# Kernel optimization log

Measured on AMD Instinct MI355X. Metric: run time of the kernel, lower is better.

Reference implementation:

```python
import jax, jax.numpy as jnp
import numpy as np

T, R, I = 16384, 1024, 128   # time steps, reservoir size, input size
CONN, SR = 0.05, 0.9         # connectivity_rate, spectral_radius


def _make_reservoir(rng):
    # Faithful to ESN.create_reservoir_weights: uniform[0,1), sparsify by
    # connectivity_rate, rescale to target spectral radius, flip half the
    # entries' signs.
    W = rng.random((R, R)).astype(np.float32)
    W[rng.random((R, R)) > CONN] = 0.0
    cur_sr = np.max(np.abs(np.linalg.eigvals(W)))
    W = W * (SR / cur_sr)
    neg = rng.choice(R * R, (R * R) // 2, replace=False)
    Wf = W.reshape(-1).copy()
    Wf[neg] *= -1.0
    return Wf.reshape(R, R).astype(np.float32)


def setup_inputs() -> dict:
    rng = np.random.default_rng(0)
    W_res = jnp.asarray(_make_reservoir(rng))
    key = jax.random.key(0)
    k1, k2 = jax.random.split(key)
    X = jax.random.normal(k1, (T, I), dtype=jnp.float32)
    # nn.init.uniform_(w, a=-1, b=1)
    W_in = jax.random.uniform(k2, (R, I), dtype=jnp.float32, minval=-1.0, maxval=1.0)
    state0 = jnp.zeros((R,), dtype=jnp.float32)
    return {"X": X, "W_in": W_in, "W_res": W_res, "state0": state0}


def reference(X, W_in, W_res, state0):
    # state_t = tanh(W_in @ x_t + W_res @ state_{t-1}); collect all states (T, R).
    # Input projections are independent across time -> one big GEMM up front.
    U = X @ W_in.T  # (T, R)

    def step(s, u):
        s = jnp.tanh(u + W_res @ s)
        return s, s

    _, all_states = jax.lax.scan(step, state0, U)
    return all_states  # (T, R), matches update_state's all_states
```

## Files before the change

kernel.cpp:

```cpp
#include <hip/hip_runtime.h>
#include <hip/hip_bf16.h>
#include <stdint.h>


constexpr int T_N = 16384;
constexpr int R_N = 1024;
constexpr int I_N = 128;

constexpr int BT = 64, BR = 64;

__global__ __launch_bounds__(256) void gemm_u_kernel(
    const float* __restrict__ X, const float* __restrict__ Win,
    float* __restrict__ U)
{
    __shared__ float XS[BT][68];
    __shared__ float WS[BR][68];
    const int tid = threadIdx.x;
    const int ty = tid >> 4, tx = tid & 15;
    const int t0 = blockIdx.x * BT;
    const int r0 = blockIdx.y * BR;
    float acc[4][4] = {};

    for (int k0 = 0; k0 < I_N; k0 += 64) {
        for (int idx = tid; idx < BT * 16; idx += 256) {
            int row = idx >> 4, c4 = (idx & 15) << 2;
            *reinterpret_cast<float4*>(&XS[row][c4]) =
                *reinterpret_cast<const float4*>(&X[(size_t)(t0 + row) * I_N + k0 + c4]);
        }
        for (int idx = tid; idx < BR * 16; idx += 256) {
            int row = idx >> 4, c4 = (idx & 15) << 2;
            *reinterpret_cast<float4*>(&WS[row][c4]) =
                *reinterpret_cast<const float4*>(&Win[(size_t)(r0 + row) * I_N + k0 + c4]);
        }
        __syncthreads();
#pragma unroll
        for (int k = 0; k < 64; k += 4) {
            float4 a[4], b[4];
#pragma unroll
            for (int i = 0; i < 4; ++i)
                a[i] = *reinterpret_cast<const float4*>(&XS[ty + 16 * i][k]);
#pragma unroll
            for (int jj = 0; jj < 4; ++jj)
                b[jj] = *reinterpret_cast<const float4*>(&WS[tx + 16 * jj][k]);
#pragma unroll
            for (int i = 0; i < 4; ++i)
#pragma unroll
                for (int jj = 0; jj < 4; ++jj)
                    acc[i][jj] += a[i].x * b[jj].x + a[i].y * b[jj].y +
                                  a[i].z * b[jj].z + a[i].w * b[jj].w;
        }
        __syncthreads();
    }
#pragma unroll
    for (int i = 0; i < 4; ++i)
#pragma unroll
        for (int jj = 0; jj < 4; ++jj)
            U[(size_t)(t0 + ty + 16 * i) * R_N + (r0 + tx + 16 * jj)] = acc[i][jj];
}

constexpr int GBLK  = 8;
constexpr int B2    = 1024;
constexpr int RPB   = R_N / GBLK;
constexpr int TPR   = 8;
constexpr int KMAX  = 96;
constexpr int NSL   = KMAX / TPR;
constexpr int DEPTH = 2;
constexpr int PCAP  = 1 << 20;

typedef unsigned long long ull;

__device__ __forceinline__ float fast_tanh(float x) {
    float ax = fabsf(x);
    float e  = __expf(-2.0f * ax);
    float y  = (1.0f - e) / (1.0f + e);
    return copysignf(y, x);
}

__global__ __launch_bounds__(1024) void esn_scan_kernel(
    const float* __restrict__ Wres, const float* __restrict__ state0,
    float* out, ull* slots)
{
    __shared__ float sbuf[DEPTH][R_N];
    __shared__ uint2 ell[RPB][KMAX];
    __shared__ int   cnt[RPB];

    const int tid  = threadIdx.x;
    const int b    = blockIdx.x;
    const int row0 = b * RPB;

    if (tid < RPB) cnt[tid] = 0;
    __syncthreads();
    for (int idx = tid; idx < RPB * R_N; idx += B2) {
        int r = idx >> 10, c = idx & (R_N - 1);
        float w = Wres[(size_t)(row0 + r) * R_N + c];
        if (w != 0.0f) {
            int slot = atomicAdd(&cnt[r], 1);
            if (slot < KMAX) ell[r][slot] = make_uint2((uint32_t)c, __float_as_uint(w));
        }
    }
    __syncthreads();

    const int rloc = tid / TPR;
    const int j    = tid % TPR;
    const int row  = row0 + rloc;
    int   cols[NSL];
    float vals[NSL];
    {
        int myn = cnt[rloc];
#pragma unroll
        for (int k = 0; k < NSL; ++k) {
            int slot = j + k * TPR;
            if (slot < myn) {
                uint2 e = ell[rloc][slot];
                cols[k] = (int)e.x;
                vals[k] = __uint_as_float(e.y);
            } else { cols[k] = 0; vals[k] = 0.0f; }
        }
    }

    sbuf[1][tid] = state0[tid];

    float u_cur = (j == 0) ? out[row] : 0.0f;
    __syncthreads();

    for (int t = 0; t < T_N; ++t) {
        const int p = (t - 1) & 1;

        float u_next = 0.0f;
        if (j == 0 && t + 1 < T_N) u_next = out[(size_t)(t + 1) * R_N + row];

        if (t > 0) {
            const ull* addr = slots + ((size_t)p << 10) + tid;
            const uint32_t want = (uint32_t)t;
            ull w;
            int rounds = 0;
            do {
                w = __hip_atomic_load(addr, __ATOMIC_RELAXED,
                                      __HIP_MEMORY_SCOPE_AGENT);
            } while ((uint32_t)(w >> 32) < want && ++rounds < PCAP);
            sbuf[p][tid] = __uint_as_float((uint32_t)w);
        }
        __syncthreads();

        float acc = 0.0f;
#pragma unroll
        for (int k = 0; k < NSL; ++k) acc += vals[k] * sbuf[p][cols[k]];

        acc += __shfl_xor(acc, 1, TPR);
        acc += __shfl_xor(acc, 2, TPR);
        acc += __shfl_xor(acc, 4, TPR);

        if (j == 0) {
            float y = fast_tanh(u_cur + acc);
            ull pkt = ((ull)(uint32_t)(t + 1) << 32) | (ull)__float_as_uint(y);
            __hip_atomic_store(&slots[((size_t)(t & 1) << 10) + row], pkt,
                               __ATOMIC_RELAXED, __HIP_MEMORY_SCOPE_AGENT);
            out[(size_t)t * R_N + row] = y;
        }
        u_cur = u_next;
    }
}

extern "C" void kernel_launch(void* const* d_in, const int* in_sizes, int n_in,
                              void* d_out, int out_size, void* d_ws, size_t ws_size,
                              hipStream_t stream)
{
    const float* X      = (const float*)d_in[0];
    const float* W_in   = (const float*)d_in[1];
    const float* W_res  = (const float*)d_in[2];
    const float* state0 = (const float*)d_in[3];
    float* out = (float*)d_out;
    ull* slots = (ull*)d_ws;

    hipMemsetAsync(d_ws, 0, (size_t)DEPTH * R_N * sizeof(ull), stream);

    dim3 g1(T_N / BT, R_N / BR);
    gemm_u_kernel<<<g1, 256, 0, stream>>>(X, W_in, out);

    esn_scan_kernel<<<GBLK, B2, 0, stream>>>(W_res, state0, out, slots);
}
```

Measured before the change: 24.27 ms.

## Co-locate scan blocks on one XCD and poll 32-bit tagged slots via L2

The scan kernel now launches 64 blocks and elects the 8 that landed on the same XCD, using the hardware XCC id, to run the recurrence. The other blocks exit. A startup probe checks whether L2 atomic-add reads see peer stores, and if so the per-step handoff polls with those reads. Slots shrink to 32 bits, with an 8-bit step tag packed into the low mantissa bits of the state. The inner sparse loop also skips padded ELL entries. The aim is to cut the per-step cross-block communication latency. The cost is a slightly truncated state value that feeds the recurrence, plus dependence on block placement, with a fallback path when co-location fails.

```diff
diff --git a/kernel.cpp b/kernel.cpp
--- a/kernel.cpp
+++ b/kernel.cpp
@@ -58,16 +58,15 @@
             U[(size_t)(t0 + ty + 16 * i) * R_N + (r0 + tx + 16 * jj)] = acc[i][jj];
 }
 
-constexpr int GBLK  = 8;
-constexpr int B2    = 1024;
-constexpr int RPB   = R_N / GBLK;
-constexpr int TPR   = 8;
-constexpr int KMAX  = 96;
-constexpr int NSL   = KMAX / TPR;
-constexpr int DEPTH = 2;
-constexpr int PCAP  = 1 << 20;
-
-typedef unsigned long long ull;
+constexpr int GBLK    = 8;
+constexpr int NLAUNCH = 64;
+constexpr int B2      = 1024;
+constexpr int RPB     = R_N / GBLK;
+constexpr int TPR     = 8;
+constexpr int KMAX    = 96;
+constexpr int NSL     = KMAX / TPR;
+constexpr int FASTCAP = 24;
+constexpr int PCAP    = 1 << 20;
 
 __device__ __forceinline__ float fast_tanh(float x) {
     float ax = fabsf(x);
@@ -76,17 +75,81 @@
     return copysignf(y, x);
 }
 
+__device__ __forceinline__ uint32_t l2_atomic_read(uint32_t* addr) {
+    uint32_t old;
+    asm volatile("global_atomic_add %0, %1, %2, off sc0\n\t"
+                 "s_waitcnt vmcnt(0)"
+                 : "=v"(old) : "v"(addr), "v"(0u) : "memory");
+    return old;
+}
+
 __global__ __launch_bounds__(1024) void esn_scan_kernel(
     const float* __restrict__ Wres, const float* __restrict__ state0,
-    float* out, ull* slots)
+    float* out, uint32_t* hdr, uint32_t* slots)
 {
-    __shared__ float sbuf[DEPTH][R_N];
+    __shared__ int   s_role, s_fast;
+    __shared__ float sbuf[2][R_N];
     __shared__ uint2 ell[RPB][KMAX];
     __shared__ int   cnt[RPB];
 
-    const int tid  = threadIdx.x;
-    const int b    = blockIdx.x;
+    const int tid = threadIdx.x;
+
+    if (tid == 0) {
+        uint32_t xcd;
+        asm volatile("s_getreg_b32 %0, hwreg(HW_REG_XCC_ID)" : "=s"(xcd));
+        xcd &= 7u;
+        uint32_t rank = __hip_atomic_fetch_add(&hdr[xcd], 1u,
+                            __ATOMIC_RELAXED, __HIP_MEMORY_SCOPE_AGENT);
+        int role = -1;
+        if (rank < (uint32_t)GBLK) {
+            if (rank == (uint32_t)(GBLK - 1)) {
+                uint32_t expected = 0u;
+                __hip_atomic_compare_exchange_strong(&hdr[8], &expected, xcd + 1u,
+                    __ATOMIC_RELAXED, __ATOMIC_RELAXED, __HIP_MEMORY_SCOPE_AGENT);
+            }
+            uint32_t win = 0; int sp = 0;
+            do {
+                win = __hip_atomic_load(&hdr[8], __ATOMIC_RELAXED,
+                                        __HIP_MEMORY_SCOPE_AGENT);
+            } while (win == 0u && ++sp < PCAP);
+            if (win == xcd + 1u) role = (int)rank;
+        }
+        s_role = role; s_fast = 0;
+    }
+    __syncthreads();
+    const int b = s_role;
+    if (b < 0) return;
     const int row0 = b * RPB;
+
+    if (tid == 0) {
+        uint32_t* test = hdr + 96;
+        if (b == 0) {
+            asm volatile("global_store_dword %0, %1, off"
+                         :: "v"(test), "v"(0xC0FFEEu) : "memory");
+            __hip_atomic_store(&hdr[9], 1u, __ATOMIC_RELAXED,
+                               __HIP_MEMORY_SCOPE_AGENT);
+        } else {
+            int sp = 0;
+            while (!__hip_atomic_load(&hdr[9], __ATOMIC_RELAXED,
+                                      __HIP_MEMORY_SCOPE_AGENT) && ++sp < PCAP) {}
+        }
+        uint32_t seen = 0;
+        for (int r = 0; r < 32 && !seen; ++r)
+            if (l2_atomic_read(test) == 0xC0FFEEu) seen = 1;
+        __hip_atomic_store(&hdr[16 + b], seen ? 1u : 2u,
+                           __ATOMIC_RELAXED, __HIP_MEMORY_SCOPE_AGENT);
+        uint32_t ok = 1;
+        for (int i = 0; i < GBLK; ++i) {
+            uint32_t v; int sp = 0;
+            do { v = __hip_atomic_load(&hdr[16 + i], __ATOMIC_RELAXED,
+                                       __HIP_MEMORY_SCOPE_AGENT);
+            } while (!v && ++sp < PCAP);
+            if (v != 1u) ok = 0;
+        }
+        s_fast = (int)ok;
+    }
+    __syncthreads();
+    const bool fastp = (s_fast != 0);
 
     if (tid < RPB) cnt[tid] = 0;
     __syncthreads();
@@ -105,8 +168,11 @@
     const int row  = row0 + rloc;
     int   cols[NSL];
     float vals[NSL];
+    int   kcnt;
     {
         int myn = cnt[rloc];
+        if (myn > KMAX) myn = KMAX;
+        kcnt = (myn > j) ? (((myn - 1 - j) >> 3) + 1) : 0;
 #pragma unroll
         for (int k = 0; k < NSL; ++k) {
             int slot = j + k * TPR;
@@ -119,7 +185,6 @@
     }
 
     sbuf[1][tid] = state0[tid];
-
     float u_cur = (j == 0) ? out[row] : 0.0f;
     __syncthreads();
 
@@ -130,21 +195,31 @@
         if (j == 0 && t + 1 < T_N) u_next = out[(size_t)(t + 1) * R_N + row];
 
         if (t > 0) {
-            const ull* addr = slots + ((size_t)p << 10) + tid;
-            const uint32_t want = (uint32_t)t;
-            ull w;
-            int rounds = 0;
-            do {
-                w = __hip_atomic_load(addr, __ATOMIC_RELAXED,
-                                      __HIP_MEMORY_SCOPE_AGENT);
-            } while ((uint32_t)(w >> 32) < want && ++rounds < PCAP);
-            sbuf[p][tid] = __uint_as_float((uint32_t)w);
+            uint32_t* addr = slots + ((size_t)p << 10) + tid;
+            const uint32_t want8 = (uint32_t)(t & 0xFF);
+            uint32_t w = 0;
+            bool got = false;
+            if (fastp) {
+                for (int r = 0; r < FASTCAP; ++r) {
+                    w = l2_atomic_read(addr);
+                    if ((w & 0xFFu) == want8) { got = true; break; }
+                }
+            }
+            if (!got) {
+                int sp = 0;
+                do {
+                    w = __hip_atomic_load(addr, __ATOMIC_RELAXED,
+                                          __HIP_MEMORY_SCOPE_AGENT);
+                } while ((w & 0xFFu) != want8 && ++sp < PCAP);
+            }
+            sbuf[p][tid] = __uint_as_float(w & 0xFFFFFF00u);
         }
         __syncthreads();
 
         float acc = 0.0f;
 #pragma unroll
-        for (int k = 0; k < NSL; ++k) acc += vals[k] * sbuf[p][cols[k]];
+        for (int k = 0; k < NSL; ++k)
+            if (k < kcnt) acc += vals[k] * sbuf[p][cols[k]];
 
         acc += __shfl_xor(acc, 1, TPR);
         acc += __shfl_xor(acc, 2, TPR);
@@ -152,7 +227,9 @@
 
         if (j == 0) {
             float y = fast_tanh(u_cur + acc);
-            ull pkt = ((ull)(uint32_t)(t + 1) << 32) | (ull)__float_as_uint(y);
+            uint32_t bits = __float_as_uint(y);
+            uint32_t pkt  = ((bits + 0x80u) & 0xFFFFFF00u)
+                          | ((uint32_t)(t + 1) & 0xFFu);
             __hip_atomic_store(&slots[((size_t)(t & 1) << 10) + row], pkt,
                                __ATOMIC_RELAXED, __HIP_MEMORY_SCOPE_AGENT);
             out[(size_t)t * R_N + row] = y;
@@ -170,12 +247,14 @@
     const float* W_res  = (const float*)d_in[2];
     const float* state0 = (const float*)d_in[3];
     float* out = (float*)d_out;
-    ull* slots = (ull*)d_ws;
-
-    hipMemsetAsync(d_ws, 0, (size_t)DEPTH * R_N * sizeof(ull), stream);
+
+    uint32_t* hdr   = (uint32_t*)d_ws;
+    uint32_t* slots = (uint32_t*)((char*)d_ws + 1024);
+
+    hipMemsetAsync(d_ws, 0, 1024 + (size_t)2 * R_N * sizeof(uint32_t), stream);
 
     dim3 g1(T_N / BT, R_N / BR);
     gemm_u_kernel<<<g1, 256, 0, stream>>>(X, W_in, out);
 
-    esn_scan_kernel<<<GBLK, B2, 0, stream>>>(W_res, state0, out, slots);
-}
+    esn_scan_kernel<<<NLAUNCH, B2, 0, stream>>>(W_res, state0, out, hdr, slots);
+}
```

Result: no change. 24.16 ms (-0.4%).

## Spread scan over 64 single-wave blocks with packed 32-bit state/epoch slots

Applied to the files above, without the earlier changes.

Splits the recurrent scan from 8 blocks of 1024 threads into 64 single-wavefront blocks, each handling 16 rows with 4 threads per row. Each exchanged state value is packed into a 32-bit word: the mantissa is rounded to free its low 8 bits, which hold a step tag. Each thread polls 16 slots per step, which halves the traffic per value and makes __syncthreads cheap with one wave per block. The cost is a small precision loss in the recurrent state that compounds over steps, plus many more blocks spinning on global memory. The ELL build is vectorised, and the dot-product loop skips empty slots.

```diff
diff --git a/kernel.cpp b/kernel.cpp
--- a/kernel.cpp
+++ b/kernel.cpp
@@ -58,16 +58,14 @@
             U[(size_t)(t0 + ty + 16 * i) * R_N + (r0 + tx + 16 * jj)] = acc[i][jj];
 }
 
-constexpr int GBLK  = 8;
-constexpr int B2    = 1024;
-constexpr int RPB   = R_N / GBLK;
-constexpr int TPR   = 8;
-constexpr int KMAX  = 96;
-constexpr int NSL   = KMAX / TPR;
-constexpr int DEPTH = 2;
-constexpr int PCAP  = 1 << 20;
-
-typedef unsigned long long ull;
+constexpr int GBLK = 64;
+constexpr int B2   = 64;
+constexpr int RPB  = R_N / GBLK;
+constexpr int TPR  = 4;
+constexpr int KMAX = 96;
+constexpr int NSL  = KMAX / TPR;
+constexpr int SPL  = R_N / B2;
+constexpr int PCAP = 1 << 20;
 
 __device__ __forceinline__ float fast_tanh(float x) {
     float ax = fabsf(x);
@@ -76,11 +74,11 @@
     return copysignf(y, x);
 }
 
-__global__ __launch_bounds__(1024) void esn_scan_kernel(
+__global__ __launch_bounds__(64) void esn_scan_kernel(
     const float* __restrict__ Wres, const float* __restrict__ state0,
-    float* out, ull* slots)
+    float* out, uint32_t* slots)
 {
-    __shared__ float sbuf[DEPTH][R_N];
+    __shared__ float sbuf[2][R_N];
     __shared__ uint2 ell[RPB][KMAX];
     __shared__ int   cnt[RPB];
 
@@ -90,26 +88,36 @@
 
     if (tid < RPB) cnt[tid] = 0;
     __syncthreads();
-    for (int idx = tid; idx < RPB * R_N; idx += B2) {
-        int r = idx >> 10, c = idx & (R_N - 1);
-        float w = Wres[(size_t)(row0 + r) * R_N + c];
-        if (w != 0.0f) {
-            int slot = atomicAdd(&cnt[r], 1);
-            if (slot < KMAX) ell[r][slot] = make_uint2((uint32_t)c, __float_as_uint(w));
+    for (int idx = tid; idx < RPB * (R_N / 4); idx += B2) {
+        int r = idx >> 8;
+        int c = (idx & 255) << 2;
+        float4 w4 = *reinterpret_cast<const float4*>(
+            &Wres[(size_t)(row0 + r) * R_N + c]);
+        float wv[4] = {w4.x, w4.y, w4.z, w4.w};
+#pragma unroll
+        for (int e = 0; e < 4; ++e) {
+            if (wv[e] != 0.0f) {
+                int slot = atomicAdd(&cnt[r], 1);
+                if (slot < KMAX)
+                    ell[r][slot] = make_uint2((uint32_t)(c + e), __float_as_uint(wv[e]));
+            }
         }
     }
     __syncthreads();
 
-    const int rloc = tid / TPR;
-    const int j    = tid % TPR;
+    const int rloc = tid >> 2;
+    const int j    = tid & 3;
     const int row  = row0 + rloc;
     int   cols[NSL];
     float vals[NSL];
+    int   kcnt;
     {
         int myn = cnt[rloc];
+        if (myn > KMAX) myn = KMAX;
+        kcnt = (myn > j) ? (((myn - 1 - j) >> 2) + 1) : 0;
 #pragma unroll
         for (int k = 0; k < NSL; ++k) {
-            int slot = j + k * TPR;
+            int slot = j + (k << 2);
             if (slot < myn) {
                 uint2 e = ell[rloc][slot];
                 cols[k] = (int)e.x;
@@ -118,8 +126,8 @@
         }
     }
 
-    sbuf[1][tid] = state0[tid];
-
+#pragma unroll
+    for (int k = 0; k < SPL; ++k) sbuf[1][(k << 6) + tid] = state0[(k << 6) + tid];
     float u_cur = (j == 0) ? out[row] : 0.0f;
     __syncthreads();
 
@@ -130,29 +138,41 @@
         if (j == 0 && t + 1 < T_N) u_next = out[(size_t)(t + 1) * R_N + row];
 
         if (t > 0) {
-            const ull* addr = slots + ((size_t)p << 10) + tid;
-            const uint32_t want = (uint32_t)t;
-            ull w;
-            int rounds = 0;
+            const uint32_t* base = slots + ((size_t)p << 10);
+            const uint32_t want8 = (uint32_t)t & 0xFFu;
+            uint32_t w[SPL];
+            int sp = 0;
+            bool fresh = false;
             do {
-                w = __hip_atomic_load(addr, __ATOMIC_RELAXED,
-                                      __HIP_MEMORY_SCOPE_AGENT);
-            } while ((uint32_t)(w >> 32) < want && ++rounds < PCAP);
-            sbuf[p][tid] = __uint_as_float((uint32_t)w);
+#pragma unroll
+                for (int k = 0; k < SPL; ++k)
+                    w[k] = __hip_atomic_load(base + (k << 6) + tid,
+                                             __ATOMIC_RELAXED,
+                                             __HIP_MEMORY_SCOPE_AGENT);
+                uint32_t bad = 0;
+#pragma unroll
+                for (int k = 0; k < SPL; ++k) bad |= (w[k] ^ want8);
+                fresh = ((bad & 0xFFu) == 0u);
+            } while (!fresh && ++sp < PCAP);
+#pragma unroll
+            for (int k = 0; k < SPL; ++k)
+                sbuf[p][(k << 6) + tid] = __uint_as_float(w[k] & 0xFFFFFF00u);
         }
         __syncthreads();
 
         float acc = 0.0f;
 #pragma unroll
-        for (int k = 0; k < NSL; ++k) acc += vals[k] * sbuf[p][cols[k]];
+        for (int k = 0; k < NSL; ++k)
+            if (k < kcnt) acc += vals[k] * sbuf[p][cols[k]];
 
         acc += __shfl_xor(acc, 1, TPR);
         acc += __shfl_xor(acc, 2, TPR);
-        acc += __shfl_xor(acc, 4, TPR);
 
         if (j == 0) {
             float y = fast_tanh(u_cur + acc);
-            ull pkt = ((ull)(uint32_t)(t + 1) << 32) | (ull)__float_as_uint(y);
+            uint32_t bits = __float_as_uint(y);
+            uint32_t pkt  = ((bits + 0x80u) & 0xFFFFFF00u)
+                          | ((uint32_t)(t + 1) & 0xFFu);
             __hip_atomic_store(&slots[((size_t)(t & 1) << 10) + row], pkt,
                                __ATOMIC_RELAXED, __HIP_MEMORY_SCOPE_AGENT);
             out[(size_t)t * R_N + row] = y;
@@ -170,9 +190,9 @@
     const float* W_res  = (const float*)d_in[2];
     const float* state0 = (const float*)d_in[3];
     float* out = (float*)d_out;
-    ull* slots = (ull*)d_ws;
-
-    hipMemsetAsync(d_ws, 0, (size_t)DEPTH * R_N * sizeof(ull), stream);
+    uint32_t* slots = (uint32_t*)d_ws;
+
+    hipMemsetAsync(d_ws, 0, (size_t)2 * R_N * sizeof(uint32_t), stream);
 
     dim3 g1(T_N / BT, R_N / BR);
     gemm_u_kernel<<<g1, 256, 0, stream>>>(X, W_in, out);
```

Result: slower. 29.84 ms (+22.9%).
